# Kernel optimization log

Hardware: AMD Instinct MI355X
Metric: run time of the kernel (lower is better)

The kernel has to match this reference:

```python
import jax, jax.numpy as jnp
import numpy as np


def hard_sigmoid(x):
    # Keras hard_sigmoid: clip(0.2*x + 0.5, 0, 1)
    return jnp.clip(x * 0.2 + 0.5, 0.0, 1.0)


def conv2d_same(x, w):
    # x: [B,H,W,Cin], w: [kh,kw,Cin,Cout]
    return jax.lax.conv_general_dilated(
        x, w, window_strides=(1, 1), padding='SAME',
        dimension_numbers=('NHWC', 'HWIO', 'NHWC'))


def convlstm2d(x, Wx, Wh, b):
    # x: [B,T,H,W,Cin]; Wx: [k,k,Cin,4*Cout]; Wh: [k,k,Cout,4*Cout]; b: [4*Cout]
    B, T, H, W, _ = x.shape
    Cout = Wh.shape[2]
    h0 = jnp.zeros((B, H, W, Cout), x.dtype)
    c0 = jnp.zeros((B, H, W, Cout), x.dtype)

    def step(carry, xt):
        h, c = carry
        z = conv2d_same(xt, Wx) + conv2d_same(h, Wh) + b
        i, f, g, o = jnp.split(z, 4, axis=-1)  # Keras gate order i,f,c,o
        c = hard_sigmoid(f) * c + hard_sigmoid(i) * jnp.tanh(g)
        h = hard_sigmoid(o) * jnp.tanh(c)
        return (h, c), h

    _, hs = jax.lax.scan(step, (h0, c0), jnp.moveaxis(x, 1, 0))
    return jnp.moveaxis(hs, 0, 1)  # [B,T,H,W,Cout]


def bn_inference(x, gamma, beta, mean, var, eps=1e-3):
    # Keras BatchNormalization default eps=1e-3, inference mode (training=False)
    return (x - mean) * jax.lax.rsqrt(var + eps) * gamma + beta


def upsample_2x2(x):
    # UpSampling3D(size=(1,2,2)) on [B,T,H,W,C]
    return jnp.repeat(jnp.repeat(x, 2, axis=2), 2, axis=3)


def deconv_block(x, Wx, Wh, b, g, be, mm, mv):
    return upsample_2x2(bn_inference(convlstm2d(x, Wx, Wh, b), g, be, mm, mv))


def setup_inputs() -> dict:
    key = jax.random.key(0)
    ks = jax.random.split(key, 32)
    B, T, H, W = 2, 8, 16, 16
    Cin = 192
    chans = [128, 64, 32]
    K = 3
    d = {'x': jax.random.normal(ks[0], (B, T, H, W, Cin), jnp.float32)}
    ci = Cin
    ki = 1
    for l, co in enumerate(chans, start=1):
        d[f'Wx{l}'] = jax.random.normal(ks[ki], (K, K, ci, 4 * co), jnp.float32) * 0.05; ki += 1
        d[f'Wh{l}'] = jax.random.normal(ks[ki], (K, K, co, 4 * co), jnp.float32) * 0.05; ki += 1
        d[f'b{l}'] = jnp.zeros((4 * co,), jnp.float32)
        d[f'g{l}'] = jax.random.uniform(ks[ki], (co,), jnp.float32) + 0.5; ki += 1
        d[f'be{l}'] = jax.random.normal(ks[ki], (co,), jnp.float32) * 0.1; ki += 1
        d[f'mm{l}'] = jax.random.normal(ks[ki], (co,), jnp.float32) * 0.1; ki += 1
        d[f'mv{l}'] = jax.random.uniform(ks[ki], (co,), jnp.float32) + 0.5; ki += 1
        ci = co
    return d


def reference(x, Wx1, Wh1, b1, g1, be1, mm1, mv1,
              Wx2, Wh2, b2, g2, be2, mm2, mv2,
              Wx3, Wh3, b3, g3, be3, mm3, mv3):
    x = deconv_block(x, Wx1, Wh1, b1, g1, be1, mm1, mv1)  # [2,8,32,32,128]
    x = deconv_block(x, Wx2, Wh2, b2, g2, be2, mm2, mv2)  # [2,8,64,64,64]
    x = deconv_block(x, Wx3, Wh3, b3, g3, be3, mm3, mv3)  # [2,8,128,128,32]
    return x
```

## Files before the change

kernel.cpp:

```cpp
#include <hip/hip_runtime.h>
#include <math.h>

#define BATCH 2
#define TSTEPS 8

typedef __attribute__((ext_vector_type(8))) short s16x8;
typedef __attribute__((ext_vector_type(4))) float f32x4;

__device__ __forceinline__ float hsig(float v){ return fminf(fmaxf(0.2f*v+0.5f,0.f),1.f); }
__device__ __forceinline__ ushort f2bf(float f){
    uint u = __builtin_bit_cast(uint, f);
    u = (u + 0x7FFFu + ((u >> 16) & 1u)) >> 16;
    return (ushort)u;
}
__device__ __forceinline__ uint pack2bf(float lo, float hi){
    return (uint)f2bf(lo) | ((uint)f2bf(hi) << 16);
}

template<int KCH, int Co>
__device__ __forceinline__ void packw(const float* __restrict__ W, ushort* __restrict__ dst, int d){
    int j = d & 7, lane = (d >> 3) & 63;
    int q = lane >> 4, l = lane & 15;
    int rest = d >> 9;
    int c = rest % KCH, t_n = rest / KCH;
    int k = c*32 + q*8 + j;
    int np = t_n*16 + l;
    int g = np & 3, co = np >> 2;
    dst[d] = f2bf(W[(size_t)k*(4*Co) + g*Co + co]);
}

#define SZ_X    786432
#define SZ_WX1  884736
#define SZ_WH1  589824
#define SZ_WX2  294912
#define SZ_WH2  147456
#define SZ_WX3  73728
#define SZ_WH3  36864
#define SZ_PREP (SZ_X+SZ_WX1+SZ_WH1+SZ_WX2+SZ_WH2+SZ_WX3+SZ_WH3)

__global__ void prep_kernel(const float* __restrict__ x,
    const float* __restrict__ Wx1, const float* __restrict__ Wh1,
    const float* __restrict__ Wx2, const float* __restrict__ Wh2,
    const float* __restrict__ Wx3, const float* __restrict__ Wh3,
    ushort* __restrict__ xpad,
    ushort* __restrict__ Wxp1, ushort* __restrict__ Whp1,
    ushort* __restrict__ Wxp2, ushort* __restrict__ Whp2,
    ushort* __restrict__ Wxp3, ushort* __restrict__ Whp3)
{
    int i = blockIdx.x * 256 + threadIdx.x;
    if (i < SZ_X){
        int c = i % 192; int r = i / 192;
        int xx = r % 16; r /= 16; int yy = r % 16; int bt = r / 16;
        xpad[((size_t)bt*18*18 + (yy+1)*18 + (xx+1))*192 + c] = f2bf(x[i]);
        return;
    } i -= SZ_X;
    if (i < SZ_WX1){ packw<54,128>(Wx1, Wxp1, i); return; } i -= SZ_WX1;
    if (i < SZ_WH1){ packw<36,128>(Wh1, Whp1, i); return; } i -= SZ_WH1;
    if (i < SZ_WX2){ packw<36, 64>(Wx2, Wxp2, i); return; } i -= SZ_WX2;
    if (i < SZ_WH2){ packw<18, 64>(Wh2, Whp2, i); return; } i -= SZ_WH2;
    if (i < SZ_WX3){ packw<18, 32>(Wx3, Wxp3, i); return; } i -= SZ_WX3;
    if (i < SZ_WH3){ packw< 9, 32>(Wh3, Whp3, i); }
}

template<int CI, int CO, int H, int W>
__global__ __launch_bounds__(256) void convx_k(
    const ushort* __restrict__ Apad, const ushort* __restrict__ Wpk,
    const float* __restrict__ bias, float* __restrict__ Zx)
{
    constexpr int W_T = (W < 32) ? W : 32;
    constexpr int ROWS = 32 / W_T;
    constexpr int PR = ROWS + 2, PPX = W_T + 2;
    constexpr int PCI = CI + 8;
    constexpr int KCH = 9*CI/32, CPT = CI/32;
    constexpr int HW = H*W, HP = H+2, WP = W+2;
    constexpr int N4 = 4*CO;
    constexpr int CH8 = CI/8;
    constexpr int TOT = PR*PPX*CH8;

    __shared__ ushort patch[PR*PPX*PCI];
    __shared__ float Zsc[32][132];

    const int tid = threadIdx.x, lane = tid & 63, wave = tid >> 6;
    const int quad = lane >> 4, l16 = lane & 15;
    const int m0 = blockIdx.x * 32;
    const int bt = m0 / HW, rem = m0 - bt*HW;
    const int y0 = rem / W, x0 = rem - (rem/W)*W;

    const ushort* gsrc = Apad + (size_t)bt*HP*WP*CI;
    for (int c = tid; c < TOT; c += 256){
        int pix = c / CH8, ch = c - pix*CH8;
        int prow = pix / PPX, ppx = pix - prow*PPX;
        *(uint4*)&patch[pix*PCI + ch*8] =
            *(const uint4*)(gsrc + ((size_t)(y0+prow)*WP + (x0+ppx))*CI + ch*8);
    }
    __syncthreads();

    const int tn0 = blockIdx.y*8 + wave*2;
    const ushort* bptr0 = Wpk + ((size_t)tn0*KCH*64 + lane)*8;
    const ushort* bptr1 = Wpk + ((size_t)(tn0+1)*KCH*64 + lane)*8;

    int labase[2];
    #pragma unroll
    for (int s = 0; s < 2; ++s){
        int p = s*16 + l16;
        int rp = p / W_T, xp = p - rp*W_T;
        labase[s] = (rp*PPX + xp)*PCI + quad*8;
    }

    f32x4 acc[2][2] = {};
    #pragma unroll
    for (int it = 0; it < KCH; ++it){
        const int tap = it / CPT, ci0 = (it - tap*CPT)*32;
        const int kh = tap/3, kw = tap - (tap/3)*3;
        const int off = (kh*PPX + kw)*PCI + ci0;
        s16x8 b0 = *(const s16x8*)(bptr0 + (size_t)it*512);
        s16x8 b1 = *(const s16x8*)(bptr1 + (size_t)it*512);
        s16x8 a0 = *(const s16x8*)&patch[labase[0] + off];
        s16x8 a1 = *(const s16x8*)&patch[labase[1] + off];
        acc[0][0] = __builtin_amdgcn_mfma_f32_16x16x32_bf16(a0, b0, acc[0][0], 0,0,0);
        acc[0][1] = __builtin_amdgcn_mfma_f32_16x16x32_bf16(a0, b1, acc[0][1], 0,0,0);
        acc[1][0] = __builtin_amdgcn_mfma_f32_16x16x32_bf16(a1, b0, acc[1][0], 0,0,0);
        acc[1][1] = __builtin_amdgcn_mfma_f32_16x16x32_bf16(a1, b1, acc[1][1], 0,0,0);
    }

    #pragma unroll
    for (int s = 0; s < 2; ++s){
        #pragma unroll
        for (int nt = 0; nt < 2; ++nt){
            const int col = blockIdx.y*128 + wave*32 + nt*16 + l16;
            const float bv = bias[(col & 3)*CO + (col >> 2)];
            #pragma unroll
            for (int r = 0; r < 4; ++r)
                Zsc[s*16 + quad*4 + r][wave*32 + nt*16 + l16] = acc[s][nt][r] + bv;
        }
    }
    __syncthreads();

    #pragma unroll
    for (int i = 0; i < 4; ++i){
        int c = i*256 + tid;
        int row = c >> 5, cc = (c & 31) << 2;
        *(float4*)&Zx[(size_t)(m0+row)*N4 + blockIdx.y*128 + cc] = *(float4*)&Zsc[row][cc];
    }
}

template<int CI, int CO, int H, int W>
__device__ __forceinline__ void conv_slice_role(char* smem, int lbid, int t,
    const ushort* __restrict__ Apad, const ushort* __restrict__ Wpk,
    const float* __restrict__ bias, float* __restrict__ Zx)
{
    constexpr int W_T = (W < 32) ? W : 32;
    constexpr int PR = (32/W_T) + 2, PPX = W_T + 2;
    constexpr int PCI = CI + 8;
    constexpr int KCH = 9*CI/32, CPT = CI/32;
    constexpr int HW = H*W, HP = H+2, WP = W+2;
    constexpr int N4 = 4*CO;
    constexpr int CH8 = CI/8;
    constexpr int TOT = PR*PPX*CH8;
    constexpr int TPB = HW/32;
    constexpr int PXT = 2*TPB;

    ushort* patch = (ushort*)smem;
    float* Zsc = (float*)(smem + PR*PPX*PCI*2);

    const int tid = threadIdx.x, lane = tid & 63, wave = tid >> 6;
    const int quad = lane >> 4, l16 = lane & 15;
    const int lx = lbid % PXT, ly = lbid / PXT;
    const int b = lx / TPB;
    const int idx0 = (lx - b*TPB)*32;
    const int bt = b*TSTEPS + t;
    const int m0 = bt*HW + idx0;
    const int y0 = idx0 / W, x0 = idx0 - (idx0/W)*W;

    const ushort* gsrc = Apad + (size_t)bt*HP*WP*CI;
    for (int c = tid; c < TOT; c += 256){
        int pix = c / CH8, ch = c - pix*CH8;
        int prow = pix / PPX, ppx = pix - prow*PPX;
        *(uint4*)&patch[pix*PCI + ch*8] =
            *(const uint4*)(gsrc + ((size_t)(y0+prow)*WP + (x0+ppx))*CI + ch*8);
    }
    __syncthreads();

    const int tn0 = ly*8 + wave*2;
    const ushort* bptr0 = Wpk + ((size_t)tn0*KCH*64 + lane)*8;
    const ushort* bptr1 = Wpk + ((size_t)(tn0+1)*KCH*64 + lane)*8;

    int labase[2];
    #pragma unroll
    for (int s = 0; s < 2; ++s){
        int p = s*16 + l16;
        int rp = p / W_T, xp = p - rp*W_T;
        labase[s] = (rp*PPX + xp)*PCI + quad*8;
    }

    f32x4 acc[2][2] = {};
    #pragma unroll
    for (int it = 0; it < KCH; ++it){
        const int tap = it / CPT, ci0 = (it - tap*CPT)*32;
        const int kh = tap/3, kw = tap - (tap/3)*3;
        const int off = (kh*PPX + kw)*PCI + ci0;
        s16x8 b0 = *(const s16x8*)(bptr0 + (size_t)it*512);
        s16x8 b1 = *(const s16x8*)(bptr1 + (size_t)it*512);
        s16x8 a0 = *(const s16x8*)&patch[labase[0] + off];
        s16x8 a1 = *(const s16x8*)&patch[labase[1] + off];
        acc[0][0] = __builtin_amdgcn_mfma_f32_16x16x32_bf16(a0, b0, acc[0][0], 0,0,0);
        acc[0][1] = __builtin_amdgcn_mfma_f32_16x16x32_bf16(a0, b1, acc[0][1], 0,0,0);
        acc[1][0] = __builtin_amdgcn_mfma_f32_16x16x32_bf16(a1, b0, acc[1][0], 0,0,0);
        acc[1][1] = __builtin_amdgcn_mfma_f32_16x16x32_bf16(a1, b1, acc[1][1], 0,0,0);
    }

    #pragma unroll
    for (int s = 0; s < 2; ++s){
        #pragma unroll
        for (int nt = 0; nt < 2; ++nt){
            const int col = ly*128 + wave*32 + nt*16 + l16;
            const float bv = bias[(col & 3)*CO + (col >> 2)];
            #pragma unroll
            for (int r = 0; r < 4; ++r)
                Zsc[(s*16 + quad*4 + r)*132 + wave*32 + nt*16 + l16] = acc[s][nt][r] + bv;
        }
    }
    __syncthreads();

    #pragma unroll
    for (int i = 0; i < 4; ++i){
        int c = i*256 + tid;
        int row = c >> 5, cc = (c & 31) << 2;
        *(float4*)&Zx[(size_t)(m0+row)*N4 + ly*128 + cc] = *(float4*)&Zsc[row*132 + cc];
    }
}

template<int CO, int H, int W, int OUT_BF16>
__device__ __forceinline__ void step_role(char* smem, int lbid, int t, int first,
    const float* __restrict__ Zx, const ushort* __restrict__ Whpk,
    const ushort* __restrict__ hprev, ushort* __restrict__ hnew,
    float* __restrict__ cst,
    const float* __restrict__ gamma, const float* __restrict__ beta,
    const float* __restrict__ mmean, const float* __restrict__ mvar,
    void* __restrict__ outp)
{
    constexpr int W_T = (W < 32) ? W : 32;
    constexpr int PR = (32/W_T) + 2, PPX = W_T + 2;
    constexpr int PCO = CO + 8;
    constexpr int KCH = 9*CO/32, CPT = CO/32;
    constexpr int NJ = (KCH + 3)/4;
    constexpr int HW = H*W, HP = H+2, WP = W+2;
    constexpr int N4 = 4*CO;
    constexpr int CH8 = CO/8;
    constexpr int TOT = PR*PPX*CH8;
    constexpr int PT = (BATCH*HW)/32;

    ushort* patch = (ushort*)smem;
    float* Zs = (float*)(smem + PR*PPX*PCO*2);
    float* Hs = (float*)(smem + PR*PPX*PCO*2 + 18432);

    const int tid = threadIdx.x, lane = tid & 63, wave = tid >> 6;
    const int quad = lane >> 4, l16 = lane & 15;
    const int pxt = lbid % PT, colIdx = lbid / PT;
    const int m0 = pxt * 32;
    const int b2 = m0 / HW, rem = m0 - b2*HW;
    const int y0 = rem / W, x0 = rem - (rem/W)*W;
    const int co0 = colIdx * 8;

    if (!first){
        const ushort* gsrc = hprev + (size_t)b2*HP*WP*CO;
        for (int c = tid; c < TOT; c += 256){
            int pix = c / CH8, ch = c - pix*CH8;
            int prow = pix / PPX, ppx = pix - prow*PPX;
            *(uint4*)&patch[pix*PCO + ch*8] =
                *(const uint4*)(gsrc + ((size_t)(y0+prow)*WP + (x0+ppx))*CO + ch*8);
        }
        __syncthreads();

        const int tn0 = colIdx*2;
        const ushort* bptr0 = Whpk + ((size_t)tn0*KCH*64 + lane)*8;
        const ushort* bptr1 = Whpk + ((size_t)(tn0+1)*KCH*64 + lane)*8;

        int labase[2];
        #pragma unroll
        for (int s = 0; s < 2; ++s){
            int p = s*16 + l16;
            int rp = p / W_T, xp = p - rp*W_T;
            labase[s] = (rp*PPX + xp)*PCO + quad*8;
        }

        f32x4 acc[2][2] = {};
        const int nj = (KCH - wave + 3) >> 2;
        #pragma unroll
        for (int j = 0; j < NJ; ++j){
            if (j < nj){
                const int it = wave + 4*j;
                const int tap = it / CPT, ci0 = (it - tap*CPT)*32;
                const int kh = tap/3, kw = tap - (tap/3)*3;
                const int off = (kh*PPX + kw)*PCO + ci0;
                s16x8 b0 = *(const s16x8*)(bptr0 + (size_t)it*512);
                s16x8 b1 = *(const s16x8*)(bptr1 + (size_t)it*512);
                s16x8 a0 = *(const s16x8*)&patch[labase[0] + off];
                s16x8 a1 = *(const s16x8*)&patch[labase[1] + off];
                acc[0][0] = __builtin_amdgcn_mfma_f32_16x16x32_bf16(a0, b0, acc[0][0], 0,0,0);
                acc[0][1] = __builtin_amdgcn_mfma_f32_16x16x32_bf16(a0, b1, acc[0][1], 0,0,0);
                acc[1][0] = __builtin_amdgcn_mfma_f32_16x16x32_bf16(a1, b0, acc[1][0], 0,0,0);
                acc[1][1] = __builtin_amdgcn_mfma_f32_16x16x32_bf16(a1, b1, acc[1][1], 0,0,0);
            }
        }
        #pragma unroll
        for (int s = 0; s < 2; ++s)
            #pragma unroll
            for (int nt = 0; nt < 2; ++nt)
                #pragma unroll
                for (int r = 0; r < 4; ++r)
                    Zs[(wave*32 + s*16 + quad*4 + r)*36 + nt*16 + l16] = acc[s][nt][r];
        __syncthreads();
    }

    {
        const int px = tid >> 3, coin = tid & 7;
        const int m = m0 + px;
        const int rr = m - b2*HW;
        const int co = co0 + coin;
        const size_t zrow = (size_t)(b2*TSTEPS + t)*HW + rr;
        const float4 zx = *(const float4*)&Zx[zrow*N4 + colIdx*32 + coin*4];
        float zi = zx.x, zf = zx.y, zg = zx.z, zo = zx.w;
        if (!first){
            #pragma unroll
            for (int w = 0; w < 4; ++w){
                const float4 s = *(const float4*)&Zs[(w*32 + px)*36 + coin*4];
                zi += s.x; zf += s.y; zg += s.z; zo += s.w;
            }
        }
        const float iv = hsig(zi), fv = hsig(zf);
        const float gv = tanhf(zg), ov = hsig(zo);
        const float cold = first ? 0.f : cst[(size_t)m*CO + co];
        const float cn = fv*cold + iv*gv;
        cst[(size_t)m*CO + co] = cn;
        const float h = ov * tanhf(cn);
        const int y = rr / W, x = rr - (rr/W)*W;
        hnew[((size_t)b2*HP*WP + (y+1)*WP + (x+1))*CO + co] = f2bf(h);
        Hs[px*8 + coin] = (h - mmean[co])*rsqrtf(mvar[co]+1e-3f)*gamma[co] + beta[co];
    }
    __syncthreads();

    if (OUT_BF16){
        if (tid < 128){
            const int px = tid >> 2, q = tid & 3;
            const int ypos = q >> 1, xpos = q & 1;
            const int m = m0 + px;
            const int rr = m - b2*HW;
            const int y = rr / W, x = rr - (rr/W)*W;
            const float* hs = &Hs[px*8];
            uint4 v;
            v.x = pack2bf(hs[0], hs[1]); v.y = pack2bf(hs[2], hs[3]);
            v.z = pack2bf(hs[4], hs[5]); v.w = pack2bf(hs[6], hs[7]);
            ushort* o = (ushort*)outp;
            const size_t opix = ((size_t)(b2*TSTEPS + t)*(2*H+2) + 2*y+1+ypos)*(size_t)(2*W+2) + 2*x+1+xpos;
            *(uint4*)&o[opix*CO + co0] = v;
        }
    } else {
        const int px = tid >> 3, q = (tid >> 1) & 3, half = tid & 1;
        const int ypos = q >> 1, xpos = q & 1;
        const int m = m0 + px;
        const int rr = m - b2*HW;
        const int y = rr / W, x = rr - (rr/W)*W;
        float4 v = *(const float4*)&Hs[px*8 + half*4];
        float* o = (float*)outp;
        const size_t opix = ((size_t)(b2*TSTEPS + t)*(2*H) + 2*y+ypos)*(size_t)(2*W) + 2*x+xpos;
        *(float4*)&o[opix*CO + co0 + half*4] = v;
    }
}

__global__ __launch_bounds__(256) void mega(
    int e1, int e2, int e3, int e4,
    int t1, int t2, int t3, int t4, int t5,
    int f1, int f2, int f3,
    const float* Zx1, const ushort* Whp1, const ushort* h1p, ushort* h1n, float* c1,
    const float* g1, const float* be1, const float* mm1, const float* mv1, ushort* x2pad,
    const ushort* Wxp2, const float* b2v, float* Zx2,
    const ushort* Whp2, const ushort* h2p, ushort* h2n, float* c2,
    const float* g2, const float* be2, const float* mm2, const float* mv2, ushort* x3pad,
    const ushort* Wxp3, const float* b3v, float* Zx3,
    const ushort* Whp3, const ushort* h3p, ushort* h3n, float* c3,
    const float* g3, const float* be3, const float* mm3, const float* mv3, float* outp)
{
    __shared__ __align__(16) char smem[44672];
    const int bid = blockIdx.x;
    if (bid < e1){
        step_role<128,16,16,1>(smem, bid, t1, f1, Zx1, Whp1, h1p, h1n, c1, g1, be1, mm1, mv1, x2pad);
        return;
    }
    if (bid < e2){
        conv_slice_role<128,64,32,32>(smem, bid - e1, t2, x2pad, Wxp2, b2v, Zx2);
        return;
    }
    if (bid < e3){
        step_role<64,32,32,1>(smem, bid - e2, t3, f2, Zx2, Whp2, h2p, h2n, c2, g2, be2, mm2, mv2, x3pad);
        return;
    }
    if (bid < e4){
        conv_slice_role<64,32,64,64>(smem, bid - e3, t4, x3pad, Wxp3, b3v, Zx3);
        return;
    }
    step_role<32,64,64,0>(smem, bid - e4, t5, f3, Zx3, Whp3, h3p, h3n, c3, g3, be3, mm3, mv3, outp);
}

extern "C" void kernel_launch(void* const* d_in, const int* in_sizes, int n_in,
                              void* d_out, int out_size, void* d_ws, size_t ws_size,
                              hipStream_t stream) {
    const float* x   = (const float*)d_in[0];
    const float* Wx1 = (const float*)d_in[1];  const float* Wh1 = (const float*)d_in[2];
    const float* b1  = (const float*)d_in[3];  const float* g1  = (const float*)d_in[4];
    const float* be1 = (const float*)d_in[5];  const float* mm1 = (const float*)d_in[6];
    const float* mv1 = (const float*)d_in[7];
    const float* Wx2 = (const float*)d_in[8];  const float* Wh2 = (const float*)d_in[9];
    const float* b2  = (const float*)d_in[10]; const float* g2  = (const float*)d_in[11];
    const float* be2 = (const float*)d_in[12]; const float* mm2 = (const float*)d_in[13];
    const float* mv2 = (const float*)d_in[14];
    const float* Wx3 = (const float*)d_in[15]; const float* Wh3 = (const float*)d_in[16];
    const float* b3  = (const float*)d_in[17]; const float* g3  = (const float*)d_in[18];
    const float* be3 = (const float*)d_in[19]; const float* mm3 = (const float*)d_in[20];
    const float* mv3 = (const float*)d_in[21];

    char* ws = (char*)d_ws;
    size_t off = 0;
    auto alloc = [&](size_t bytes) { char* p = ws + off; off += (bytes + 255) & ~(size_t)255; return p; };

    float*  Zx1 = (float*)alloc(2097152ull * 4);
    float*  Zx2 = (float*)alloc(4194304ull * 4);
    float*  Zx3 = (float*)alloc(8388608ull * 4);
    float*  c1  = (float*)alloc(65536ull * 4);
    float*  c2  = (float*)alloc(131072ull * 4);
    float*  c3  = (float*)alloc(262144ull * 4);

    char* zbase = alloc(17685504ull);
    ushort* xpad  = (ushort*)zbase;
    ushort* x2pad = xpad  + 995328;
    ushort* x3pad = x2pad + 2367488;
    ushort* h1A   = x3pad + 4460544;
    ushort* h1B   = h1A + 82944;
    ushort* h2A   = h1B + 82944;
    ushort* h2B   = h2A + 147968;
    ushort* h3A   = h2B + 147968;
    ushort* h3B   = h3A + 278784;

    ushort* Wxp1 = (ushort*)alloc(884736ull * 2);
    ushort* Wxp2 = (ushort*)alloc(294912ull * 2);
    ushort* Wxp3 = (ushort*)alloc(73728ull * 2);
    ushort* Whp1 = (ushort*)alloc(589824ull * 2);
    ushort* Whp2 = (ushort*)alloc(147456ull * 2);
    ushort* Whp3 = (ushort*)alloc(36864ull * 2);

    hipMemsetAsync(zbase, 0, 17685504ull, stream);

    prep_kernel<<<(SZ_PREP + 255) / 256, 256, 0, stream>>>(
        x, Wx1, Wh1, Wx2, Wh2, Wx3, Wh3,
        xpad, Wxp1, Whp1, Wxp2, Whp2, Wxp3, Whp3);

    convx_k<192, 128, 16, 16><<<dim3(128, 4), 256, 0, stream>>>(xpad, Wxp1, b1, Zx1);

    for (int j = 0; j < 12; ++j){
        const int a1 = (j < 8),            t1 = a1 ? j     : 0;
        const int a2 = (j >= 1 && j <= 8), tc2 = a2 ? j - 1 : 0;
        const int a3 = (j >= 2 && j <= 9), ts2 = a3 ? j - 2 : 0;
        const int a4 = (j >= 3 && j <= 10), tc3 = a4 ? j - 3 : 0;
        const int a5 = (j >= 4),           ts3 = a5 ? j - 4 : 0;

        const int e1 = a1 ? 256 : 0;
        const int e2 = e1 + (a2 ? 128 : 0);
        const int e3 = e2 + (a3 ? 512 : 0);
        const int e4 = e3 + (a4 ? 256 : 0);
        const int e5 = e4 + (a5 ? 1024 : 0);
        if (e5 == 0) continue;

        const ushort* h1p = (t1 & 1) ? h1B : h1A;  ushort* h1n = (t1 & 1) ? h1A : h1B;
        const ushort* h2p = (ts2 & 1) ? h2B : h2A; ushort* h2n = (ts2 & 1) ? h2A : h2B;
        const ushort* h3p = (ts3 & 1) ? h3B : h3A; ushort* h3n = (ts3 & 1) ? h3A : h3B;

        mega<<<dim3(e5), 256, 0, stream>>>(
            e1, e2, e3, e4,
            t1, tc2, ts2, tc3, ts3,
            (t1 == 0), (ts2 == 0), (ts3 == 0),
            Zx1, Whp1, h1p, h1n, c1, g1, be1, mm1, mv1, x2pad,
            Wxp2, b2, Zx2,
            Whp2, h2p, h2n, c2, g2, be2, mm2, mv2, x3pad,
            Wxp3, b3, Zx3,
            Whp3, h3p, h3n, c3, g3, be3, mm3, mv3, (float*)d_out);
    }
}
```

Before: 281.9 us.

## Fuse input and recurrent convolutions for layers 2-3 and reschedule the pipeline

For layers 2 and 3, the separate input-convolution slices that wrote fp32 Zx buffers are removed. Each step block now loads both the x patch and the h patch and runs one combined K loop over concatenated packed weights, so the large Zx2/Zx3 round trips through global memory go away. Layer 1's input convolution is folded into the mega kernel one timestep ahead, and the wavefront needs fewer launches (10 instead of 12 plus a separate conv launch). Shared memory is aliased between patch and Z scratch to lower LDS use, at the cost of more work per step block on the recurrent critical path.

```diff
diff --git a/kernel.cpp b/kernel.cpp
--- a/kernel.cpp
+++ b/kernel.cpp
@@ -29,14 +29,29 @@
     dst[d] = f2bf(W[(size_t)k*(4*Co) + g*Co + co]);
 }
 
+template<int CPX, int CPH, int CI, int CO>
+__device__ __forceinline__ void packw_fused(const float* __restrict__ Wx, const float* __restrict__ Wh,
+                                            ushort* __restrict__ dst, int d){
+    constexpr int KCHc = 9*(CPX+CPH);
+    int j = d & 7, lane = (d >> 3) & 63;
+    int q = lane >> 4, l = lane & 15;
+    int rest = d >> 9;
+    int c = rest % KCHc, t_n = rest / KCHc;
+    int tap = c/(CPX+CPH), u = c - tap*(CPX+CPH);
+    int np = t_n*16 + l;
+    int g = np & 3, co = np >> 2;
+    float v;
+    if (u < CPX) v = Wx[(size_t)(tap*CI + u*32 + q*8 + j)*(4*CO) + g*CO + co];
+    else         v = Wh[(size_t)(tap*CO + (u-CPX)*32 + q*8 + j)*(4*CO) + g*CO + co];
+    dst[d] = f2bf(v);
+}
+
 #define SZ_X    786432
 #define SZ_WX1  884736
 #define SZ_WH1  589824
-#define SZ_WX2  294912
-#define SZ_WH2  147456
-#define SZ_WX3  73728
-#define SZ_WH3  36864
-#define SZ_PREP (SZ_X+SZ_WX1+SZ_WH1+SZ_WX2+SZ_WH2+SZ_WX3+SZ_WH3)
+#define SZ_WC2  442368
+#define SZ_WC3  110592
+#define SZ_PREP (SZ_X+SZ_WX1+SZ_WH1+SZ_WC2+SZ_WC3)
 
 __global__ void prep_kernel(const float* __restrict__ x,
     const float* __restrict__ Wx1, const float* __restrict__ Wh1,
@@ -44,8 +59,7 @@
     const float* __restrict__ Wx3, const float* __restrict__ Wh3,
     ushort* __restrict__ xpad,
     ushort* __restrict__ Wxp1, ushort* __restrict__ Whp1,
-    ushort* __restrict__ Wxp2, ushort* __restrict__ Whp2,
-    ushort* __restrict__ Wxp3, ushort* __restrict__ Whp3)
+    ushort* __restrict__ Wc2, ushort* __restrict__ Wc3)
 {
     int i = blockIdx.x * 256 + threadIdx.x;
     if (i < SZ_X){
@@ -56,35 +70,34 @@
     } i -= SZ_X;
     if (i < SZ_WX1){ packw<54,128>(Wx1, Wxp1, i); return; } i -= SZ_WX1;
     if (i < SZ_WH1){ packw<36,128>(Wh1, Whp1, i); return; } i -= SZ_WH1;
-    if (i < SZ_WX2){ packw<36, 64>(Wx2, Wxp2, i); return; } i -= SZ_WX2;
-    if (i < SZ_WH2){ packw<18, 64>(Wh2, Whp2, i); return; } i -= SZ_WH2;
-    if (i < SZ_WX3){ packw<18, 32>(Wx3, Wxp3, i); return; } i -= SZ_WX3;
-    if (i < SZ_WH3){ packw< 9, 32>(Wh3, Whp3, i); }
-}
-
-template<int CI, int CO, int H, int W>
-__global__ __launch_bounds__(256) void convx_k(
+    if (i < SZ_WC2){ packw_fused<4,2,128,64>(Wx2, Wh2, Wc2, i); return; } i -= SZ_WC2;
+    if (i < SZ_WC3){ packw_fused<2,1,64,32>(Wx3, Wh3, Wc3, i); }
+}
+
+__device__ __forceinline__ void conv1_role(char* smem, int lbid, int t,
     const ushort* __restrict__ Apad, const ushort* __restrict__ Wpk,
     const float* __restrict__ bias, float* __restrict__ Zx)
 {
-    constexpr int W_T = (W < 32) ? W : 32;
-    constexpr int ROWS = 32 / W_T;
-    constexpr int PR = ROWS + 2, PPX = W_T + 2;
-    constexpr int PCI = CI + 8;
-    constexpr int KCH = 9*CI/32, CPT = CI/32;
+    constexpr int CI = 192, H = 16, W = 16;
+    constexpr int PR = 4, PPX = 18, PCI = CI + 8;
+    constexpr int KCH = 54, CPT = 6;
     constexpr int HW = H*W, HP = H+2, WP = W+2;
-    constexpr int N4 = 4*CO;
+    constexpr int N4 = 512;
     constexpr int CH8 = CI/8;
     constexpr int TOT = PR*PPX*CH8;
-
-    __shared__ ushort patch[PR*PPX*PCI];
-    __shared__ float Zsc[32][132];
+    constexpr int TPB = HW/32;
+
+    ushort* patch = (ushort*)smem;
+    float* Zsc = (float*)smem;
 
     const int tid = threadIdx.x, lane = tid & 63, wave = tid >> 6;
     const int quad = lane >> 4, l16 = lane & 15;
-    const int m0 = blockIdx.x * 32;
-    const int bt = m0 / HW, rem = m0 - bt*HW;
-    const int y0 = rem / W, x0 = rem - (rem/W)*W;
+    const int lx = lbid % (2*TPB), ly = lbid / (2*TPB);
+    const int b = lx / TPB;
+    const int idx0 = (lx - b*TPB)*32;
+    const int bt = b*TSTEPS + t;
+    const int m0 = bt*HW + idx0;
+    const int y0 = idx0 / W, x0 = 0;
 
     const ushort* gsrc = Apad + (size_t)bt*HP*WP*CI;
     for (int c = tid; c < TOT; c += 256){
@@ -95,17 +108,14 @@
     }
     __syncthreads();
 
-    const int tn0 = blockIdx.y*8 + wave*2;
+    const int tn0 = ly*8 + wave*2;
     const ushort* bptr0 = Wpk + ((size_t)tn0*KCH*64 + lane)*8;
     const ushort* bptr1 = Wpk + ((size_t)(tn0+1)*KCH*64 + lane)*8;
 
     int labase[2];
     #pragma unroll
-    for (int s = 0; s < 2; ++s){
-        int p = s*16 + l16;
-        int rp = p / W_T, xp = p - rp*W_T;
-        labase[s] = (rp*PPX + xp)*PCI + quad*8;
-    }
+    for (int s = 0; s < 2; ++s)
+        labase[s] = (s*PPX + l16)*PCI + quad*8;
 
     f32x4 acc[2][2] = {};
     #pragma unroll
@@ -122,99 +132,14 @@
         acc[1][0] = __builtin_amdgcn_mfma_f32_16x16x32_bf16(a1, b0, acc[1][0], 0,0,0);
         acc[1][1] = __builtin_amdgcn_mfma_f32_16x16x32_bf16(a1, b1, acc[1][1], 0,0,0);
     }
-
-    #pragma unroll
-    for (int s = 0; s < 2; ++s){
-        #pragma unroll
-        for (int nt = 0; nt < 2; ++nt){
-            const int col = blockIdx.y*128 + wave*32 + nt*16 + l16;
-            const float bv = bias[(col & 3)*CO + (col >> 2)];
-            #pragma unroll
-            for (int r = 0; r < 4; ++r)
-                Zsc[s*16 + quad*4 + r][wave*32 + nt*16 + l16] = acc[s][nt][r] + bv;
-        }
-    }
-    __syncthreads();
-
-    #pragma unroll
-    for (int i = 0; i < 4; ++i){
-        int c = i*256 + tid;
-        int row = c >> 5, cc = (c & 31) << 2;
-        *(float4*)&Zx[(size_t)(m0+row)*N4 + blockIdx.y*128 + cc] = *(float4*)&Zsc[row][cc];
-    }
-}
-
-template<int CI, int CO, int H, int W>
-__device__ __forceinline__ void conv_slice_role(char* smem, int lbid, int t,
-    const ushort* __restrict__ Apad, const ushort* __restrict__ Wpk,
-    const float* __restrict__ bias, float* __restrict__ Zx)
-{
-    constexpr int W_T = (W < 32) ? W : 32;
-    constexpr int PR = (32/W_T) + 2, PPX = W_T + 2;
-    constexpr int PCI = CI + 8;
-    constexpr int KCH = 9*CI/32, CPT = CI/32;
-    constexpr int HW = H*W, HP = H+2, WP = W+2;
-    constexpr int N4 = 4*CO;
-    constexpr int CH8 = CI/8;
-    constexpr int TOT = PR*PPX*CH8;
-    constexpr int TPB = HW/32;
-    constexpr int PXT = 2*TPB;
-
-    ushort* patch = (ushort*)smem;
-    float* Zsc = (float*)(smem + PR*PPX*PCI*2);
-
-    const int tid = threadIdx.x, lane = tid & 63, wave = tid >> 6;
-    const int quad = lane >> 4, l16 = lane & 15;
-    const int lx = lbid % PXT, ly = lbid / PXT;
-    const int b = lx / TPB;
-    const int idx0 = (lx - b*TPB)*32;
-    const int bt = b*TSTEPS + t;
-    const int m0 = bt*HW + idx0;
-    const int y0 = idx0 / W, x0 = idx0 - (idx0/W)*W;
-
-    const ushort* gsrc = Apad + (size_t)bt*HP*WP*CI;
-    for (int c = tid; c < TOT; c += 256){
-        int pix = c / CH8, ch = c - pix*CH8;
-        int prow = pix / PPX, ppx = pix - prow*PPX;
-        *(uint4*)&patch[pix*PCI + ch*8] =
-            *(const uint4*)(gsrc + ((size_t)(y0+prow)*WP + (x0+ppx))*CI + ch*8);
-    }
-    __syncthreads();
-
-    const int tn0 = ly*8 + wave*2;
-    const ushort* bptr0 = Wpk + ((size_t)tn0*KCH*64 + lane)*8;
-    const ushort* bptr1 = Wpk + ((size_t)(tn0+1)*KCH*64 + lane)*8;
-
-    int labase[2];
-    #pragma unroll
-    for (int s = 0; s < 2; ++s){
-        int p = s*16 + l16;
-        int rp = p / W_T, xp = p - rp*W_T;
-        labase[s] = (rp*PPX + xp)*PCI + quad*8;
-    }
-
-    f32x4 acc[2][2] = {};
-    #pragma unroll
-    for (int it = 0; it < KCH; ++it){
-        const int tap = it / CPT, ci0 = (it - tap*CPT)*32;
-        const int kh = tap/3, kw = tap - (tap/3)*3;
-        const int off = (kh*PPX + kw)*PCI + ci0;
-        s16x8 b0 = *(const s16x8*)(bptr0 + (size_t)it*512);
-        s16x8 b1 = *(const s16x8*)(bptr1 + (size_t)it*512);
-        s16x8 a0 = *(const s16x8*)&patch[labase[0] + off];
-        s16x8 a1 = *(const s16x8*)&patch[labase[1] + off];
-        acc[0][0] = __builtin_amdgcn_mfma_f32_16x16x32_bf16(a0, b0, acc[0][0], 0,0,0);
-        acc[0][1] = __builtin_amdgcn_mfma_f32_16x16x32_bf16(a0, b1, acc[0][1], 0,0,0);
-        acc[1][0] = __builtin_amdgcn_mfma_f32_16x16x32_bf16(a1, b0, acc[1][0], 0,0,0);
-        acc[1][1] = __builtin_amdgcn_mfma_f32_16x16x32_bf16(a1, b1, acc[1][1], 0,0,0);
-    }
+    __syncthreads();
 
     #pragma unroll
     for (int s = 0; s < 2; ++s){
         #pragma unroll
         for (int nt = 0; nt < 2; ++nt){
             const int col = ly*128 + wave*32 + nt*16 + l16;
-            const float bv = bias[(col & 3)*CO + (col >> 2)];
+            const float bv = bias[(col & 3)*128 + (col >> 2)];
             #pragma unroll
             for (int r = 0; r < 4; ++r)
                 Zsc[(s*16 + quad*4 + r)*132 + wave*32 + nt*16 + l16] = acc[s][nt][r] + bv;
@@ -230,36 +155,41 @@
     }
 }
 
-template<int CO, int H, int W, int OUT_BF16>
-__device__ __forceinline__ void step_role(char* smem, int lbid, int t, int first,
+__global__ __launch_bounds__(256) void conv1_t0(
+    const ushort* __restrict__ Apad, const ushort* __restrict__ Wpk,
+    const float* __restrict__ bias, float* __restrict__ Zx)
+{
+    __shared__ __align__(16) char smem[28800];
+    conv1_role(smem, blockIdx.x, 0, Apad, Wpk, bias, Zx);
+}
+
+__device__ __forceinline__ void step1_role(char* smem, int lbid, int t, int first,
     const float* __restrict__ Zx, const ushort* __restrict__ Whpk,
     const ushort* __restrict__ hprev, ushort* __restrict__ hnew,
     float* __restrict__ cst,
     const float* __restrict__ gamma, const float* __restrict__ beta,
     const float* __restrict__ mmean, const float* __restrict__ mvar,
-    void* __restrict__ outp)
+    ushort* __restrict__ outp)
 {
-    constexpr int W_T = (W < 32) ? W : 32;
-    constexpr int PR = (32/W_T) + 2, PPX = W_T + 2;
-    constexpr int PCO = CO + 8;
-    constexpr int KCH = 9*CO/32, CPT = CO/32;
-    constexpr int NJ = (KCH + 3)/4;
+    constexpr int CO = 128, H = 16, W = 16;
+    constexpr int PR = 4, PPX = 18, PCO = CO + 8;
+    constexpr int KCH = 36, CPT = 4, NJ = 9;
     constexpr int HW = H*W, HP = H+2, WP = W+2;
-    constexpr int N4 = 4*CO;
+    constexpr int N4 = 512;
     constexpr int CH8 = CO/8;
     constexpr int TOT = PR*PPX*CH8;
     constexpr int PT = (BATCH*HW)/32;
 
     ushort* patch = (ushort*)smem;
-    float* Zs = (float*)(smem + PR*PPX*PCO*2);
-    float* Hs = (float*)(smem + PR*PPX*PCO*2 + 18432);
+    float* Zs = (float*)smem;
+    float* Hs = (float*)(smem + 18432);
 
     const int tid = threadIdx.x, lane = tid & 63, wave = tid >> 6;
     const int quad = lane >> 4, l16 = lane & 15;
     const int pxt = lbid % PT, colIdx = lbid / PT;
     const int m0 = pxt * 32;
     const int b2 = m0 / HW, rem = m0 - b2*HW;
-    const int y0 = rem / W, x0 = rem - (rem/W)*W;
+    const int y0 = rem / W, x0 = 0;
     const int co0 = colIdx * 8;
 
     if (!first){
@@ -278,31 +208,26 @@
 
         int labase[2];
         #pragma unroll
-        for (int s = 0; s < 2; ++s){
-            int p = s*16 + l16;
-            int rp = p / W_T, xp = p - rp*W_T;
-            labase[s] = (rp*PPX + xp)*PCO + quad*8;
-        }
+        for (int s = 0; s < 2; ++s)
+            labase[s] = (s*PPX + l16)*PCO + quad*8;
 
         f32x4 acc[2][2] = {};
-        const int nj = (KCH - wave + 3) >> 2;
         #pragma unroll
         for (int j = 0; j < NJ; ++j){
-            if (j < nj){
-                const int it = wave + 4*j;
-                const int tap = it / CPT, ci0 = (it - tap*CPT)*32;
-                const int kh = tap/3, kw = tap - (tap/3)*3;
-                const int off = (kh*PPX + kw)*PCO + ci0;
-                s16x8 b0 = *(const s16x8*)(bptr0 + (size_t)it*512);
-                s16x8 b1 = *(const s16x8*)(bptr1 + (size_t)it*512);
-                s16x8 a0 = *(const s16x8*)&patch[labase[0] + off];
-                s16x8 a1 = *(const s16x8*)&patch[labase[1] + off];
-                acc[0][0] = __builtin_amdgcn_mfma_f32_16x16x32_bf16(a0, b0, acc[0][0], 0,0,0);
-                acc[0][1] = __builtin_amdgcn_mfma_f32_16x16x32_bf16(a0, b1, acc[0][1], 0,0,0);
-                acc[1][0] = __builtin_amdgcn_mfma_f32_16x16x32_bf16(a1, b0, acc[1][0], 0,0,0);
-                acc[1][1] = __builtin_amdgcn_mfma_f32_16x16x32_bf16(a1, b1, acc[1][1], 0,0,0);
-            }
-        }
+            const int it = wave + 4*j;
+            const int tap = it / CPT, ci0 = (it - tap*CPT)*32;
+            const int kh = tap/3, kw = tap - (tap/3)*3;
+            const int off = (kh*PPX + kw)*PCO + ci0;
+            s16x8 b0 = *(const s16x8*)(bptr0 + (size_t)it*512);
+            s16x8 b1 = *(const s16x8*)(bptr1 + (size_t)it*512);
+            s16x8 a0 = *(const s16x8*)&patch[labase[0] + off];
+            s16x8 a1 = *(const s16x8*)&patch[labase[1] + off];
+            acc[0][0] = __builtin_amdgcn_mfma_f32_16x16x32_bf16(a0, b0, acc[0][0], 0,0,0);
+            acc[0][1] = __builtin_amdgcn_mfma_f32_16x16x32_bf16(a0, b1, acc[0][1], 0,0,0);
+            acc[1][0] = __builtin_amdgcn_mfma_f32_16x16x32_bf16(a1, b0, acc[1][0], 0,0,0);
+            acc[1][1] = __builtin_amdgcn_mfma_f32_16x16x32_bf16(a1, b1, acc[1][1], 0,0,0);
+        }
+        __syncthreads();
         #pragma unroll
         for (int s = 0; s < 2; ++s)
             #pragma unroll
@@ -340,66 +265,203 @@
     }
     __syncthreads();
 
+    if (tid < 128){
+        const int px = tid >> 2, q = tid & 3;
+        const int ypos = q >> 1, xpos = q & 1;
+        const int m = m0 + px;
+        const int rr = m - b2*HW;
+        const int y = rr / W, x = rr - (rr/W)*W;
+        const float* hs = &Hs[px*8];
+        uint4 v;
+        v.x = pack2bf(hs[0], hs[1]); v.y = pack2bf(hs[2], hs[3]);
+        v.z = pack2bf(hs[4], hs[5]); v.w = pack2bf(hs[6], hs[7]);
+        const size_t opix = ((size_t)(b2*TSTEPS + t)*(2*H+2) + 2*y+1+ypos)*(size_t)(2*W+2) + 2*x+1+xpos;
+        *(uint4*)&outp[opix*CO + co0] = v;
+    }
+}
+
+template<int CI, int CO, int H, int W, int OUT_BF16>
+__device__ __forceinline__ void stepf_role(char* smem, int lbid, int t, int first,
+    const ushort* __restrict__ xsrc, const ushort* __restrict__ Wcp,
+    const ushort* __restrict__ hprev, ushort* __restrict__ hnew,
+    float* __restrict__ cst, const float* __restrict__ bias,
+    const float* __restrict__ gamma, const float* __restrict__ beta,
+    const float* __restrict__ mmean, const float* __restrict__ mvar,
+    void* __restrict__ outp)
+{
+    constexpr int CPX = CI/32, CPH = CO/32, CPC = CPX+CPH;
+    constexpr int KCH = 9*CPC;
+    constexpr int NJ = (KCH + 3)/4;
+    constexpr int PPX = 18;
+    constexpr int PCIx = CI + 8, PCOh = CO + 8;
+    constexpr int HW = H*W, HP = H+2, WP = W+2;
+    constexpr int XT = W/16;
+    constexpr int TPS = HW/32;
+    constexpr int CHX = CI/8, CHH = CO/8;
+    constexpr int TOTX = 72*CHX, TOTH = 72*CHH;
+
+    ushort* xpatch = (ushort*)smem;
+    ushort* hpatch = (ushort*)(smem + 4*PPX*PCIx*2);
+    float* Zs = (float*)smem;
+    float* Hs = (float*)(smem + 18432);
+
+    const int tid = threadIdx.x, lane = tid & 63, wave = tid >> 6;
+    const int quad = lane >> 4, l16 = lane & 15;
+    const int pxt = lbid % (BATCH*TPS), colIdx = lbid / (BATCH*TPS);
+    const int b2 = pxt / TPS, tau = pxt - b2*TPS;
+    const int band = tau / XT, xt = tau - band*XT;
+    const int y0 = band*2, x0 = xt*16;
+    const int co0 = colIdx * 8;
+    const int bt = b2*TSTEPS + t;
+
+    {
+        const ushort* gx = xsrc + (size_t)bt*HP*WP*CI;
+        for (int c = tid; c < TOTX; c += 256){
+            int pix = c / CHX, ch = c - pix*CHX;
+            int prow = pix / PPX, ppx = pix - prow*PPX;
+            *(uint4*)&xpatch[pix*PCIx + ch*8] =
+                *(const uint4*)(gx + ((size_t)(y0+prow)*WP + (x0+ppx))*CI + ch*8);
+        }
+    }
+    if (!first){
+        const ushort* gh = hprev + (size_t)b2*HP*WP*CO;
+        for (int c = tid; c < TOTH; c += 256){
+            int pix = c / CHH, ch = c - pix*CHH;
+            int prow = pix / PPX, ppx = pix - prow*PPX;
+            *(uint4*)&hpatch[pix*PCOh + ch*8] =
+                *(const uint4*)(gh + ((size_t)(y0+prow)*WP + (x0+ppx))*CO + ch*8);
+        }
+    }
+    __syncthreads();
+
+    const int tn0 = colIdx*2;
+    const ushort* bptr0 = Wcp + ((size_t)tn0*KCH*64 + lane)*8;
+    const ushort* bptr1 = Wcp + ((size_t)(tn0+1)*KCH*64 + lane)*8;
+
+    int labX[2], labH[2];
+    #pragma unroll
+    for (int s = 0; s < 2; ++s){
+        labX[s] = (s*PPX + l16)*PCIx + quad*8;
+        labH[s] = (s*PPX + l16)*PCOh + quad*8;
+    }
+
+    f32x4 acc[2][2] = {};
+    const int nj = (KCH - wave + 3) >> 2;
+    #pragma unroll
+    for (int j = 0; j < NJ; ++j){
+        if (j < nj){
+            const int it = wave + 4*j;
+            const int tap = it / CPC, u = it - tap*CPC;
+            if (!(first && u >= CPX)){
+                const int kh = tap/3, kw = tap - (tap/3)*3;
+                s16x8 b0 = *(const s16x8*)(bptr0 + (size_t)it*512);
+                s16x8 b1 = *(const s16x8*)(bptr1 + (size_t)it*512);
+                s16x8 a0, a1;
+                if (u < CPX){
+                    const int off = (kh*PPX + kw)*PCIx + u*32;
+                    a0 = *(const s16x8*)&xpatch[labX[0] + off];
+                    a1 = *(const s16x8*)&xpatch[labX[1] + off];
+                } else {
+                    const int off = (kh*PPX + kw)*PCOh + (u-CPX)*32;
+                    a0 = *(const s16x8*)&hpatch[labH[0] + off];
+                    a1 = *(const s16x8*)&hpatch[labH[1] + off];
+                }
+                acc[0][0] = __builtin_amdgcn_mfma_f32_16x16x32_bf16(a0, b0, acc[0][0], 0,0,0);
+                acc[0][1] = __builtin_amdgcn_mfma_f32_16x16x32_bf16(a0, b1, acc[0][1], 0,0,0);
+                acc[1][0] = __builtin_amdgcn_mfma_f32_16x16x32_bf16(a1, b0, acc[1][0], 0,0,0);
+                acc[1][1] = __builtin_amdgcn_mfma_f32_16x16x32_bf16(a1, b1, acc[1][1], 0,0,0);
+            }
+        }
+    }
+    __syncthreads();
+
+    #pragma unroll
+    for (int s = 0; s < 2; ++s)
+        #pragma unroll
+        for (int nt = 0; nt < 2; ++nt)
+            #pragma unroll
+            for (int r = 0; r < 4; ++r)
+                Zs[(wave*32 + s*16 + quad*4 + r)*36 + nt*16 + l16] = acc[s][nt][r];
+    __syncthreads();
+
+    {
+        const int px = tid >> 3, coin = tid & 7;
+        const int y = y0 + (px >> 4), x = x0 + (px & 15);
+        const int m = b2*HW + y*W + x;
+        const int co = co0 + coin;
+        float zi = bias[co], zf = bias[CO + co], zg = bias[2*CO + co], zo = bias[3*CO + co];
+        #pragma unroll
+        for (int w = 0; w < 4; ++w){
+            const float4 s = *(const float4*)&Zs[(w*32 + px)*36 + coin*4];
+            zi += s.x; zf += s.y; zg += s.z; zo += s.w;
+        }
+        const float iv = hsig(zi), fv = hsig(zf);
+        const float gv = tanhf(zg), ov = hsig(zo);
+        const float cold = first ? 0.f : cst[(size_t)m*CO + co];
+        const float cn = fv*cold + iv*gv;
+        cst[(size_t)m*CO + co] = cn;
+        const float h = ov * tanhf(cn);
+        hnew[((size_t)b2*HP*WP + (y+1)*WP + (x+1))*CO + co] = f2bf(h);
+        Hs[px*8 + coin] = (h - mmean[co])*rsqrtf(mvar[co]+1e-3f)*gamma[co] + beta[co];
+    }
+    __syncthreads();
+
     if (OUT_BF16){
         if (tid < 128){
             const int px = tid >> 2, q = tid & 3;
             const int ypos = q >> 1, xpos = q & 1;
-            const int m = m0 + px;
-            const int rr = m - b2*HW;
-            const int y = rr / W, x = rr - (rr/W)*W;
+            const int y = y0 + (px >> 4), x = x0 + (px & 15);
             const float* hs = &Hs[px*8];
             uint4 v;
             v.x = pack2bf(hs[0], hs[1]); v.y = pack2bf(hs[2], hs[3]);
             v.z = pack2bf(hs[4], hs[5]); v.w = pack2bf(hs[6], hs[7]);
             ushort* o = (ushort*)outp;
-            const size_t opix = ((size_t)(b2*TSTEPS + t)*(2*H+2) + 2*y+1+ypos)*(size_t)(2*W+2) + 2*x+1+xpos;
+            const size_t opix = ((size_t)bt*(2*H+2) + 2*y+1+ypos)*(size_t)(2*W+2) + 2*x+1+xpos;
             *(uint4*)&o[opix*CO + co0] = v;
         }
     } else {
         const int px = tid >> 3, q = (tid >> 1) & 3, half = tid & 1;
         const int ypos = q >> 1, xpos = q & 1;
-        const int m = m0 + px;
-        const int rr = m - b2*HW;
-        const int y = rr / W, x = rr - (rr/W)*W;
+        const int y = y0 + (px >> 4), x = x0 + (px & 15);
         float4 v = *(const float4*)&Hs[px*8 + half*4];
         float* o = (float*)outp;
-        const size_t opix = ((size_t)(b2*TSTEPS + t)*(2*H) + 2*y+ypos)*(size_t)(2*W) + 2*x+xpos;
+        const size_t opix = ((size_t)bt*(2*H) + 2*y+ypos)*(size_t)(2*W) + 2*x+xpos;
         *(float4*)&o[opix*CO + co0 + half*4] = v;
     }
 }
 
 __global__ __launch_bounds__(256) void mega(
-    int e1, int e2, int e3, int e4,
-    int t1, int t2, int t3, int t4, int t5,
+    int e1, int e2, int e3,
+    int t_s2, int t_s3, int t_s1, int t_c1,
     int f1, int f2, int f3,
-    const float* Zx1, const ushort* Whp1, const ushort* h1p, ushort* h1n, float* c1,
+    const ushort* xpad, const ushort* Wxp1, const float* b1v, float* Zx1,
+    const ushort* Whp1, const ushort* h1p, ushort* h1n, float* c1,
     const float* g1, const float* be1, const float* mm1, const float* mv1, ushort* x2pad,
-    const ushort* Wxp2, const float* b2v, float* Zx2,
-    const ushort* Whp2, const ushort* h2p, ushort* h2n, float* c2,
+    const ushort* Wc2, const float* b2v,
+    const ushort* h2p, ushort* h2n, float* c2,
     const float* g2, const float* be2, const float* mm2, const float* mv2, ushort* x3pad,
-    const ushort* Wxp3, const float* b3v, float* Zx3,
-    const ushort* Whp3, const ushort* h3p, ushort* h3n, float* c3,
+    const ushort* Wc3, const float* b3v,
+    const ushort* h3p, ushort* h3n, float* c3,
     const float* g3, const float* be3, const float* mm3, const float* mv3, float* outp)
 {
-    __shared__ __align__(16) char smem[44672];
+    __shared__ __align__(16) char smem[29952];
     const int bid = blockIdx.x;
     if (bid < e1){
-        step_role<128,16,16,1>(smem, bid, t1, f1, Zx1, Whp1, h1p, h1n, c1, g1, be1, mm1, mv1, x2pad);
+        stepf_role<128,64,32,32,1>(smem, bid, t_s2, f2, x2pad, Wc2, h2p, h2n, c2,
+                                   b2v, g2, be2, mm2, mv2, x3pad);
         return;
     }
     if (bid < e2){
-        conv_slice_role<128,64,32,32>(smem, bid - e1, t2, x2pad, Wxp2, b2v, Zx2);
+        stepf_role<64,32,64,64,0>(smem, bid - e1, t_s3, f3, x3pad, Wc3, h3p, h3n, c3,
+                                  b3v, g3, be3, mm3, mv3, outp);
         return;
     }
     if (bid < e3){
-        step_role<64,32,32,1>(smem, bid - e2, t3, f2, Zx2, Whp2, h2p, h2n, c2, g2, be2, mm2, mv2, x3pad);
+        step1_role(smem, bid - e2, t_s1, f1, Zx1, Whp1, h1p, h1n, c1,
+                   g1, be1, mm1, mv1, x2pad);
         return;
     }
-    if (bid < e4){
-        conv_slice_role<64,32,64,64>(smem, bid - e3, t4, x3pad, Wxp3, b3v, Zx3);
-        return;
-    }
-    step_role<32,64,64,0>(smem, bid - e4, t5, f3, Zx3, Whp3, h3p, h3n, c3, g3, be3, mm3, mv3, outp);
+    conv1_role(smem, bid - e3, t_c1, xpad, Wxp1, b1v, Zx1);
 }
 
 extern "C" void kernel_launch(void* const* d_in, const int* in_sizes, int n_in,
@@ -424,8 +486,6 @@
     auto alloc = [&](size_t bytes) { char* p = ws + off; off += (bytes + 255) & ~(size_t)255; return p; };
 
     float*  Zx1 = (float*)alloc(2097152ull * 4);
-    float*  Zx2 = (float*)alloc(4194304ull * 4);
-    float*  Zx3 = (float*)alloc(8388608ull * 4);
     float*  c1  = (float*)alloc(65536ull * 4);
     float*  c2  = (float*)alloc(131072ull * 4);
     float*  c3  = (float*)alloc(262144ull * 4);
@@ -441,47 +501,42 @@
     ushort* h3A   = h2B + 147968;
     ushort* h3B   = h3A + 278784;
 
-    ushort* Wxp1 = (ushort*)alloc(884736ull * 2);
-    ushort* Wxp2 = (ushort*)alloc(294912ull * 2);
-    ushort* Wxp3 = (ushort*)alloc(73728ull * 2);
-    ushort* Whp1 = (ushort*)alloc(589824ull * 2);
-    ushort* Whp2 = (ushort*)alloc(147456ull * 2);
-    ushort* Whp3 = (ushort*)alloc(36864ull * 2);
+    ushort* Wxp1 = (ushort*)alloc(SZ_WX1 * 2ull);
+    ushort* Whp1 = (ushort*)alloc(SZ_WH1 * 2ull);
+    ushort* Wc2  = (ushort*)alloc(SZ_WC2 * 2ull);
+    ushort* Wc3  = (ushort*)alloc(SZ_WC3 * 2ull);
 
     hipMemsetAsync(zbase, 0, 17685504ull, stream);
 
     prep_kernel<<<(SZ_PREP + 255) / 256, 256, 0, stream>>>(
         x, Wx1, Wh1, Wx2, Wh2, Wx3, Wh3,
-        xpad, Wxp1, Whp1, Wxp2, Whp2, Wxp3, Whp3);
-
-    convx_k<192, 128, 16, 16><<<dim3(128, 4), 256, 0, stream>>>(xpad, Wxp1, b1, Zx1);
-
-    for (int j = 0; j < 12; ++j){
-        const int a1 = (j < 8),            t1 = a1 ? j     : 0;
-        const int a2 = (j >= 1 && j <= 8), tc2 = a2 ? j - 1 : 0;
-        const int a3 = (j >= 2 && j <= 9), ts2 = a3 ? j - 2 : 0;
-        const int a4 = (j >= 3 && j <= 10), tc3 = a4 ? j - 3 : 0;
-        const int a5 = (j >= 4),           ts3 = a5 ? j - 4 : 0;
-
-        const int e1 = a1 ? 256 : 0;
-        const int e2 = e1 + (a2 ? 128 : 0);
-        const int e3 = e2 + (a3 ? 512 : 0);
-        const int e4 = e3 + (a4 ? 256 : 0);
-        const int e5 = e4 + (a5 ? 1024 : 0);
-        if (e5 == 0) continue;
-
-        const ushort* h1p = (t1 & 1) ? h1B : h1A;  ushort* h1n = (t1 & 1) ? h1A : h1B;
-        const ushort* h2p = (ts2 & 1) ? h2B : h2A; ushort* h2n = (ts2 & 1) ? h2A : h2B;
-        const ushort* h3p = (ts3 & 1) ? h3B : h3A; ushort* h3n = (ts3 & 1) ? h3A : h3B;
-
-        mega<<<dim3(e5), 256, 0, stream>>>(
-            e1, e2, e3, e4,
-            t1, tc2, ts2, tc3, ts3,
-            (t1 == 0), (ts2 == 0), (ts3 == 0),
-            Zx1, Whp1, h1p, h1n, c1, g1, be1, mm1, mv1, x2pad,
-            Wxp2, b2, Zx2,
-            Whp2, h2p, h2n, c2, g2, be2, mm2, mv2, x3pad,
-            Wxp3, b3, Zx3,
-            Whp3, h3p, h3n, c3, g3, be3, mm3, mv3, (float*)d_out);
-    }
-}
+        xpad, Wxp1, Whp1, Wc2, Wc3);
+
+    conv1_t0<<<64, 256, 0, stream>>>(xpad, Wxp1, b1, Zx1);
+
+    for (int j = 0; j < 10; ++j){
+        const int a_s2 = (j >= 1 && j <= 8), t_s2 = a_s2 ? j - 1 : 0;
+        const int a_s3 = (j >= 2),           t_s3 = a_s3 ? j - 2 : 0;
+        const int a_s1 = (j <= 7),           t_s1 = a_s1 ? j     : 0;
+        const int a_c1 = (j <= 6),           t_c1 = a_c1 ? j + 1 : 0;
+
+        const int e1 = a_s2 ? 512 : 0;
+        const int e2 = e1 + (a_s3 ? 1024 : 0);
+        const int e3 = e2 + (a_s1 ? 256 : 0);
+        const int e4 = e3 + (a_c1 ? 64 : 0);
+        if (e4 == 0) continue;
+
+        const ushort* h1p = (t_s1 & 1) ? h1B : h1A;  ushort* h1n = (t_s1 & 1) ? h1A : h1B;
+        const ushort* h2p = (t_s2 & 1) ? h2B : h2A;  ushort* h2n = (t_s2 & 1) ? h2A : h2B;
+        const ushort* h3p = (t_s3 & 1) ? h3B : h3A;  ushort* h3n = (t_s3 & 1) ? h3A : h3B;
+
+        mega<<<dim3(e4), 256, 0, stream>>>(
+            e1, e2, e3,
+            t_s2, t_s3, t_s1, t_c1,
+            (t_s1 == 0), (t_s2 == 0), (t_s3 == 0),
+            xpad, Wxp1, b1, Zx1,
+            Whp1, h1p, h1n, c1, g1, be1, mm1, mv1, x2pad,
+            Wc2, b2, h2p, h2n, c2, g2, be2, mm2, mv2, x3pad,
+            Wc3, b3, h3p, h3n, c3, g3, be3, mm3, mv3, (float*)d_out);
+    }
+}
```

Measured after the change: 342.3 us. 21.4% more time.
